# Optimization experiments

Hardware: AMD Instinct MI355X
Metric: run time of the kernel (lower is better)

The kernel has to match this reference:

```python
import jax, jax.numpy as jnp
import numpy as np

N_NODES = 20000   # N
N_EDGES = 320000  # E (avg degree 16)
T_STEPS = 16      # T
IN_FEATS = 1      # F
HG = 64           # hidden_g
HT = 128          # hidden_t
LN_EPS = 1e-5


def _layer_norm(x, g, b):
    mu = jnp.mean(x, axis=-1, keepdims=True)
    var = jnp.mean((x - mu) ** 2, axis=-1, keepdims=True)
    return (x - mu) * jax.lax.rsqrt(var + LN_EPS) * g + b


def setup_inputs() -> dict:
    key = jax.random.key(0)
    k = jax.random.split(key, 16)
    r = lambda i, shape, s: jax.random.normal(k[i], shape, jnp.float32) * s
    return dict(
        x_seq=jax.random.normal(k[0], (1, T_STEPS, N_NODES, IN_FEATS), jnp.float32),
        edge_index=jax.random.randint(k[1], (2, N_EDGES), 0, N_NODES, dtype=jnp.int32),
        # SAGEConv layer 0: lin_l (aggregated neighbors, has bias) + lin_r (root)
        W_l0=r(2, (IN_FEATS, HG), 0.5), W_r0=r(3, (IN_FEATS, HG), 0.5), b0=jnp.zeros((HG,), jnp.float32),
        ln0_g=jnp.ones((HG,), jnp.float32), ln0_b=jnp.zeros((HG,), jnp.float32),
        # SAGEConv layer 1
        W_l1=r(4, (HG, HG), 0.1), W_r1=r(5, (HG, HG), 0.1), b1=jnp.zeros((HG,), jnp.float32),
        ln1_g=jnp.ones((HG,), jnp.float32), ln1_b=jnp.zeros((HG,), jnp.float32),
        # GRU (torch layout: gates r,z,n stacked along first dim)
        gru_Wih=r(6, (3 * HT, HG), 0.05), gru_Whh=r(7, (3 * HT, HT), 0.05),
        gru_bih=jnp.zeros((3 * HT,), jnp.float32), gru_bhh=jnp.zeros((3 * HT,), jnp.float32),
        # head
        head_W=r(8, (HT, 1), 0.05), head_b=jnp.zeros((1,), jnp.float32),
    )


def reference(x_seq, edge_index, W_l0, W_r0, b0, ln0_g, ln0_b,
              W_l1, W_r1, b1, ln1_g, ln1_b,
              gru_Wih, gru_Whh, gru_bih, gru_bhh, head_W, head_b):
    src, dst = edge_index[0], edge_index[1]
    # in-degree for mean aggregation (clamped to 1, like PyG mean aggr on isolated nodes)
    deg = jnp.clip(jax.ops.segment_sum(jnp.ones((N_EDGES,), jnp.float32), dst,
                                       num_segments=N_NODES), 1.0)[:, None]

    def sage(x, Wl, Wr, b):
        # mean over incoming neighbors, then lin_l(aggr) + lin_r(root)
        agg = jax.ops.segment_sum(x[src], dst, num_segments=N_NODES) / deg
        return agg @ Wl + x @ Wr + b

    def stack(xt):  # xt: (N, F) -> (N, HG); dropout is identity in eval mode
        h = jax.nn.relu(_layer_norm(sage(xt, W_l0, W_r0, b0), ln0_g, ln0_b))
        h = jax.nn.relu(_layer_norm(sage(h, W_l1, W_r1, b1), ln1_g, ln1_b))
        return h

    X = x_seq[0]  # (T, N, F), B == 1
    # scan over timesteps (matches the per-t Python loop, bounds peak memory)
    _, H = jax.lax.scan(lambda c, xt: (c, stack(xt)), None, X)  # H: (T, N, HG)

    def gru_step(h, xt):  # torch GRU cell; batch = N nodes
        gi = xt @ gru_Wih.T + gru_bih
        gh = h @ gru_Whh.T + gru_bhh
        ir, iz, inn = jnp.split(gi, 3, axis=-1)
        hr, hz, hn = jnp.split(gh, 3, axis=-1)
        r = jax.nn.sigmoid(ir + hr)
        z = jax.nn.sigmoid(iz + hz)
        n = jnp.tanh(inn + r * hn)
        return (1.0 - z) * n + z * h, None

    h0 = jnp.zeros((N_NODES, HT), x_seq.dtype)
    hT, _ = jax.lax.scan(gru_step, h0, H)
    y = (hT @ head_W + head_b)[:, 0]  # (N,)
    return y
```

## Files before the change

### kernel.cpp

```cpp
#include <hip/hip_runtime.h>
#include <math.h>

#define NN 20000
#define NE 320000
#define TS 16
#define HG 64
#define HTT 128
#define NG 384
#define LN_EPS 1e-5f

typedef __attribute__((ext_vector_type(8))) _Float16 f16x8;
typedef __attribute__((ext_vector_type(4))) _Float16 f16x4;
typedef __attribute__((ext_vector_type(2))) _Float16 f16x2;
typedef __attribute__((ext_vector_type(4))) float f32x4;

__device__ __forceinline__ float wave_sum64(float v) {
  #pragma unroll
  for (int off = 32; off > 0; off >>= 1) v += __shfl_xor(v, off, 64);
  return v;
}
__device__ __forceinline__ float quad_sum16(float v) {
  #pragma unroll
  for (int off = 1; off < 16; off <<= 1) v += __shfl_xor(v, off, 64);
  return v;
}
__device__ __forceinline__ float fast_sigmoid(float x) {
  return __builtin_amdgcn_rcpf(1.f + __expf(-x));
}
__device__ __forceinline__ float fast_tanh(float x) {
  float e = __expf(-2.f * fabsf(x));
  float th = (1.f - e) * __builtin_amdgcn_rcpf(1.f + e);
  return copysignf(th, x);
}

__global__ __launch_bounds__(256) void k_setup(
    const float* __restrict__ x_seq, float* __restrict__ xT,
    const float* __restrict__ Wih, _Float16* __restrict__ WihF,
    const float* __restrict__ Whh, _Float16* __restrict__ WhhF,
    const float* __restrict__ Wl1, const float* __restrict__ Wr1,
    _Float16* __restrict__ Wchi, _Float16* __restrict__ Wclo,
    const float* __restrict__ Wl0, const float* __restrict__ Wr0,
    const float* __restrict__ b0, const float* __restrict__ g0,
    const float* __restrict__ be0, float* __restrict__ P,
    int* __restrict__ cnt) {
  int gid = blockIdx.x * 256 + threadIdx.x;
  int stride = gridDim.x * 256;
  for (int i = gid; i < NN * TS; i += stride) {
    int t = i / NN, n = i - t * NN;
    xT[n * 16 + t] = x_seq[i];
  }
  for (int i = gid; i < NG * HG; i += stride) WihF[i] = (_Float16)Wih[i];
  for (int i = gid; i < NG * HTT; i += stride) WhhF[i] = (_Float16)Whh[i];
  for (int i = gid; i < HG * 128; i += stride) {
    int n = i >> 7, k = i & 127;
    float x = (k < HG) ? Wl1[k * HG + n] : Wr1[(k - HG) * HG + n];
    _Float16 h = (_Float16)x;
    Wchi[i] = h;
    Wclo[i] = (_Float16)(x - (float)h);
  }
  for (int i = gid; i < NN; i += stride) cnt[i] = 0;
  if (blockIdx.x == 0 && threadIdx.x < 64) {
    int f = threadIdx.x;
    float u = Wl0[f], v = Wr0[f], c = b0[f], g = g0[f];
    float um = wave_sum64(u) * (1.f / 64.f);
    float vm = wave_sum64(v) * (1.f / 64.f);
    float cm = wave_sum64(c) * (1.f / 64.f);
    float uc = u - um, vc = v - vm, cc = c - cm;
    float muu = wave_sum64(uc * uc) * (1.f / 64.f);
    float mvv = wave_sum64(vc * vc) * (1.f / 64.f);
    float mcc = wave_sum64(cc * cc) * (1.f / 64.f);
    float muv = wave_sum64(uc * vc) * (1.f / 64.f);
    float muc = wave_sum64(uc * cc) * (1.f / 64.f);
    float mvc = wave_sum64(vc * cc) * (1.f / 64.f);
    P[f] = uc * g; P[64 + f] = vc * g; P[128 + f] = cc * g; P[192 + f] = be0[f];
    if (f == 0) {
      P[256] = muu; P[257] = mvv; P[258] = mcc;
      P[259] = muv; P[260] = muc; P[261] = mvc;
    }
  }
}

__global__ void k_hist(const int* __restrict__ dst, int* cnt) {
  int e = blockIdx.x * blockDim.x + threadIdx.x;
  if (e < NE) atomicAdd(&cnt[dst[e]], 1);
}

__global__ void k_scan(int* cnt, int* row_ptr, float* deg_inv) {
  __shared__ int s[1024];
  const int PER = 20;
  int tid = threadIdx.x;
  int base = tid * PER;
  int vloc[PER], dloc[PER];
  int sum = 0;
  #pragma unroll
  for (int j = 0; j < PER; j++) {
    int n = base + j;
    int d = (n < NN) ? cnt[n] : 0;
    vloc[j] = sum;
    dloc[j] = d;
    sum += d;
  }
  s[tid] = sum;
  __syncthreads();
  for (int off = 1; off < 1024; off <<= 1) {
    int t = (tid >= off) ? s[tid - off] : 0;
    __syncthreads();
    s[tid] += t;
    __syncthreads();
  }
  int excl = s[tid] - sum;
  #pragma unroll
  for (int j = 0; j < PER; j++) {
    int n = base + j;
    if (n < NN) {
      int rp = excl + vloc[j];
      row_ptr[n] = rp;
      cnt[n] = rp;
      int d = dloc[j];
      deg_inv[n] = 1.0f / (float)((d > 1) ? d : 1);
    }
  }
  if (tid == 1023) row_ptr[NN] = s[1023];
}

__global__ void k_fill(const int* __restrict__ src, const int* __restrict__ dst,
                       int* cursor, int* col) {
  int e = blockIdx.x * blockDim.x + threadIdx.x;
  if (e < NE) {
    int p = atomicAdd(&cursor[dst[e]], 1);
    col[p] = src[e];
  }
}

__global__ __launch_bounds__(256) void k_h0_fused(
    const float* __restrict__ xT,
    const int* __restrict__ row_ptr, const int* __restrict__ col,
    const float* __restrict__ deg_inv,
    const float* __restrict__ P,
    _Float16* __restrict__ h0r,
    _Float16* __restrict__ code2) {
  int lane = threadIdx.x & 63;
  int n = blockIdx.x * 4 + (threadIdx.x >> 6);
  int grp = lane >> 4, tl = lane & 15;
  int beg = row_ptr[n];
  int deg = row_ptr[n + 1] - beg;
  float s0 = 0.f, s1 = 0.f;
  int iters = (deg + 7) >> 3;
  for (int it = 0; it < iters; it++) {
    int e0 = it * 8 + grp, e1 = it * 8 + 4 + grp;
    bool v0 = e0 < deg, v1 = e1 < deg;
    int i0 = v0 ? e0 : 0, i1 = v1 ? e1 : 0;
    int c0 = col[beg + i0];
    int c1 = col[beg + i1];
    float x0 = xT[c0 * 16 + tl];
    float x1 = xT[c1 * 16 + tl];
    s0 += v0 ? x0 : 0.f;
    s1 += v1 ? x1 : 0.f;
  }
  float s = s0 + s1;
  s += __shfl_xor(s, 16, 64);
  s += __shfl_xor(s, 32, 64);
  float aggv = s * deg_inv[n];
  float xv = xT[n * 16 + tl];
  float muu = P[256], mvv = P[257], mcc = P[258];
  float muv = P[259], muc = P[260], mvc = P[261];
  if (lane < 16) {
    float a = aggv, x = xv;
    float var = a * a * muu + x * x * mvv + mcc
              + 2.f * (a * x * muv + a * muc + x * mvc);
    float rstd = rsqrtf(var + LN_EPS);
    _Float16 Ah = (_Float16)(a * rstd);
    _Float16 Xh = (_Float16)(x * rstd);
    _Float16 Ch = (_Float16)rstd;
    f16x8 cw = {Ah, Ah, Xh, Xh, Ch, Ch, (_Float16)0.f, (_Float16)0.f};
    *(f16x8*)&code2[(size_t)n * 128 + (lane & 7) * 16 + (lane >> 3) * 8] = cw;
  }
  #pragma unroll
  for (int half = 0; half < 2; half++) {
    int c = lane + half * 64;
    int t = c >> 3, f8 = (c & 7) * 8;
    float a = __shfl(aggv, t, 64);
    float x = __shfl(xv, t, 64);
    float var = a * a * muu + x * x * mvv + mcc
              + 2.f * (a * x * muv + a * muc + x * mvc);
    float rstd = rsqrtf(var + LN_EPS);
    f16x8 o;
    #pragma unroll
    for (int j = 0; j < 8; j++) {
      int f = f8 + j;
      float d = a * P[f] + x * P[64 + f] + P[128 + f];
      o[j] = (_Float16)fmaxf(d * rstd + P[192 + f], 0.f);
    }
    *(f16x8*)&h0r[(size_t)n * 1024 + c * 8] = o;
  }
}

__global__ __launch_bounds__(256) void k_gather(
    const int* __restrict__ row_ptr, const int* __restrict__ col,
    const _Float16* __restrict__ code2,
    const float* __restrict__ P,
    _Float16* __restrict__ agg) {
  int lane = threadIdx.x & 63;
  int n = blockIdx.x * 4 + (threadIdx.x >> 6);
  const f16x2 h2z = {(_Float16)0.f, (_Float16)0.f};
  const f16x2 h2o = {(_Float16)1.f, (_Float16)1.f};
  int f1 = (lane & 7) * 8;
  int tmod = lane >> 3;
  f16x2 Pu2[4], Pv2[4], Pc2[4], Pb2[4];
  #pragma unroll
  for (int j = 0; j < 4; j++) {
    Pu2[j] = (f16x2){(_Float16)P[f1 + 2*j],       (_Float16)P[f1 + 2*j + 1]};
    Pv2[j] = (f16x2){(_Float16)P[64 + f1 + 2*j],  (_Float16)P[64 + f1 + 2*j + 1]};
    Pc2[j] = (f16x2){(_Float16)P[128 + f1 + 2*j], (_Float16)P[128 + f1 + 2*j + 1]};
    Pb2[j] = (f16x2){(_Float16)P[192 + f1 + 2*j], (_Float16)P[192 + f1 + 2*j + 1]};
  }
  int beg = row_ptr[n];
  int deg = row_ptr[n + 1] - beg;
  int cvAll = (lane < deg) ? col[beg + lane] : 0;

  f16x2 aE1[4], aO1[4], aE2[4], aO2[4];
  #pragma unroll
  for (int j = 0; j < 4; j++) { aE1[j] = h2z; aO1[j] = h2z; aE2[j] = h2z; aO2[j] = h2z; }

#define ACC_SET(c, mk, FULL, ACC)                                          \
  { f16x2 _A = __builtin_shufflevector(c, c, 0, 1);                        \
    f16x2 _X = __builtin_shufflevector(c, c, 2, 3);                        \
    f16x2 _C = __builtin_shufflevector(c, c, 4, 5);                        \
    _Pragma("unroll")                                                      \
    for (int j = 0; j < 4; j++) {                                          \
      f16x2 d = __builtin_elementwise_fma(_A, Pu2[j],                      \
                 __builtin_elementwise_fma(_X, Pv2[j],                     \
                  __builtin_elementwise_fma(_C, Pc2[j], Pb2[j])));         \
      d = __builtin_elementwise_max(d, h2z);                               \
      ACC[j] = (FULL) ? (ACC[j] + d)                                       \
                      : __builtin_elementwise_fma(d, mk, ACC[j]);          \
    } }

  int nb4 = (deg + 3) >> 2;
  if (nb4 > 16) nb4 = 16;
  for (int b = 0; b < nb4; b++) {
    int eb = b << 2;
    f16x8 cA[4], cB[4];
    #pragma unroll
    for (int e = 0; e < 4; e++) {
      int c = __builtin_amdgcn_readlane(cvAll, eb + e);
      const _Float16* cp = code2 + (size_t)c * 128 + tmod * 16;
      cA[e] = *(const f16x8*)cp;
      cB[e] = *(const f16x8*)(cp + 8);
    }
    if (eb + 4 <= deg) {
      #pragma unroll
      for (int e = 0; e < 4; e++) {
        if (e & 1) { ACC_SET(cA[e], h2o, true, aO1) ACC_SET(cB[e], h2o, true, aO2) }
        else       { ACC_SET(cA[e], h2o, true, aE1) ACC_SET(cB[e], h2o, true, aE2) }
      }
    } else {
      #pragma unroll
      for (int e = 0; e < 4; e++) {
        f16x2 mk = ((eb + e) < deg) ? h2o : h2z;
        if (e & 1) { ACC_SET(cA[e], mk, false, aO1) ACC_SET(cB[e], mk, false, aO2) }
        else       { ACC_SET(cA[e], mk, false, aE1) ACC_SET(cB[e], mk, false, aE2) }
      }
    }
  }
  for (int e = 64; e < deg; e++) {
    int c = col[beg + e];
    const _Float16* cp = code2 + (size_t)c * 128 + tmod * 16;
    f16x8 ca = *(const f16x8*)cp;
    f16x8 cb = *(const f16x8*)(cp + 8);
    ACC_SET(ca, h2o, true, aE1) ACC_SET(cb, h2o, true, aE2)
  }
#undef ACC_SET

  float dif = 1.0f / (float)((deg > 1) ? deg : 1);
  _Float16 dih = (_Float16)dif;
  f16x2 di2 = {dih, dih};
  union { f16x8 v; f16x2 h[4]; } u0, u1;
  #pragma unroll
  for (int j = 0; j < 4; j++) {
    u0.h[j] = (aE1[j] + aO1[j]) * di2;
    u1.h[j] = (aE2[j] + aO2[j]) * di2;
  }
  *(f16x8*)&agg[(size_t)n * 1024 + lane * 8] = u0.v;
  *(f16x8*)&agg[(size_t)n * 1024 + 512 + lane * 8] = u1.v;
}

__global__ __launch_bounds__(256) void k_gemm(
    const _Float16* __restrict__ h0r,
    const _Float16* __restrict__ agg,
    const _Float16* __restrict__ Wchi, const _Float16* __restrict__ Wclo,
    const float* __restrict__ b1, const float* __restrict__ g1, const float* __restrict__ be1,
    _Float16* __restrict__ Ht_all) {
  int tid = threadIdx.x;
  int lane = tid & 63, wave = tid >> 6;
  int col16 = lane & 15, quad = lane >> 4;
  int m0 = blockIdx.x * 16;

  float bias[4], gg[4], bb[4];
  #pragma unroll
  for (int nt = 0; nt < 4; nt++) {
    int nf = nt * 16 + col16;
    bias[nt] = b1[nf]; gg[nt] = g1[nf]; bb[nt] = be1[nf];
  }
  size_t rowbase = (size_t)(m0 + col16) * 1024;

  for (int ts = 0; ts < 4; ts++) {
    int t = wave * 4 + ts;
    f32x4 acc[4];
    #pragma unroll
    for (int nt = 0; nt < 4; nt++) acc[nt] = (f32x4){0.f, 0.f, 0.f, 0.f};

    f16x8 aa[2], ar[2];
    #pragma unroll
    for (int kk = 0; kk < 2; kk++) {
      aa[kk] = *(const f16x8*)&agg[rowbase + t * 64 + kk * 32 + quad * 8];
      ar[kk] = *(const f16x8*)&h0r[rowbase + t * 64 + kk * 32 + quad * 8];
    }
    #pragma unroll
    for (int kk = 0; kk < 2; kk++) {
      #pragma unroll
      for (int nt = 0; nt < 4; nt++) {
        int nf = nt * 16 + col16;
        f16x8 bh = *(const f16x8*)&Wchi[nf * 128 + kk * 32 + quad * 8];
        f16x8 bl = *(const f16x8*)&Wclo[nf * 128 + kk * 32 + quad * 8];
        acc[nt] = __builtin_amdgcn_mfma_f32_16x16x32_f16(aa[kk], bh, acc[nt], 0, 0, 0);
        acc[nt] = __builtin_amdgcn_mfma_f32_16x16x32_f16(aa[kk], bl, acc[nt], 0, 0, 0);
      }
    }
    #pragma unroll
    for (int kk = 0; kk < 2; kk++) {
      #pragma unroll
      for (int nt = 0; nt < 4; nt++) {
        int nf = nt * 16 + col16;
        f16x8 bh = *(const f16x8*)&Wchi[nf * 128 + 64 + kk * 32 + quad * 8];
        f16x8 bl = *(const f16x8*)&Wclo[nf * 128 + 64 + kk * 32 + quad * 8];
        acc[nt] = __builtin_amdgcn_mfma_f32_16x16x32_f16(ar[kk], bh, acc[nt], 0, 0, 0);
        acc[nt] = __builtin_amdgcn_mfma_f32_16x16x32_f16(ar[kk], bl, acc[nt], 0, 0, 0);
      }
    }

    #pragma unroll
    for (int r = 0; r < 4; r++) {
      float v[4];
      #pragma unroll
      for (int nt = 0; nt < 4; nt++) v[nt] = acc[nt][r] + bias[nt];
      float s = (v[0] + v[1]) + (v[2] + v[3]);
      float mu = quad_sum16(s) * (1.f / 64.f);
      float sq = 0.f;
      #pragma unroll
      for (int nt = 0; nt < 4; nt++) { v[nt] -= mu; sq += v[nt] * v[nt]; }
      float var = quad_sum16(sq) * (1.f / 64.f);
      float rstd = rsqrtf(var + LN_EPS);
      int m = m0 + quad * 4 + r;
      size_t base = ((size_t)t * NN + m) * HG;
      #pragma unroll
      for (int nt = 0; nt < 4; nt++) {
        float o = fmaxf(v[nt] * rstd * gg[nt] + bb[nt], 0.f);
        Ht_all[base + nt * 16 + col16] = (_Float16)o;
      }
    }
  }
}

__global__ __launch_bounds__(256, 2) void k_gru_all(
    const _Float16* __restrict__ Ht_all,
    const _Float16* __restrict__ WihF,
    const _Float16* __restrict__ WhhF,
    const float* __restrict__ bih, const float* __restrict__ bhh,
    const float* __restrict__ headW, const float* __restrict__ headb,
    float* __restrict__ out) {
  __shared__ _Float16 WihL[NG * 64];
  __shared__ _Float16 hL[2][32 * 128];
  __shared__ float yL[4][32];

  int tid = threadIdx.x;
  int lane = tid & 63, wave = tid >> 6;
  int col16 = lane & 15, quad = lane >> 4;
  int m0 = blockIdx.x * 32;
  int gb = 2 * wave;

  for (int i = tid; i < NG * 8; i += 256) {
    int g = i >> 3, k8 = i & 7;
    *(f16x8*)&WihL[g * 64 + ((k8 + g) & 7) * 8] = *(const f16x8*)&WihF[g * 64 + k8 * 8];
  }
  for (int i = tid; i < 2 * 32 * 128; i += 256) hL[0][i] = (_Float16)0.f;

  int gts[6];
  #pragma unroll
  for (int t6 = 0; t6 < 6; t6++)
    gts[t6] = (t6 < 2) ? (gb + t6) : (t6 < 4) ? (8 + gb + t6 - 2) : (16 + gb + t6 - 4);

  f16x8 wgh[4][6];
  #pragma unroll
  for (int kk = 0; kk < 4; kk++)
    #pragma unroll
    for (int t6 = 0; t6 < 6; t6++)
      wgh[kk][t6] = *(const f16x8*)&WhhF[(size_t)(gts[t6] * 16 + col16) * HTT + kk * 32 + quad * 8];

  int jj[2]; float bR[2], bZ[2], bNi[2], bNh[2], hw[2];
  int waddr[2][4][2];
  #pragma unroll
  for (int js = 0; js < 2; js++) {
    int j = (gb + js) * 16 + col16;
    jj[js] = j;
    bR[js]  = bih[j] + bhh[j];
    bZ[js]  = bih[HTT + j] + bhh[HTT + j];
    bNi[js] = bih[2 * HTT + j];
    bNh[js] = bhh[2 * HTT + j];
    hw[js]  = headW[j];
    #pragma unroll
    for (int mt = 0; mt < 2; mt++)
      #pragma unroll
      for (int r = 0; r < 4; r++) {
        int row = mt * 16 + quad * 4 + r;
        waddr[mt][r][js] = row * 128 + (((j >> 3) + row) & 15) * 8 + (j & 7);
      }
  }
  float hreg[2][4][2];
  #pragma unroll
  for (int mt = 0; mt < 2; mt++)
    #pragma unroll
    for (int r = 0; r < 4; r++) { hreg[mt][r][0] = 0.f; hreg[mt][r][1] = 0.f; }

  size_t aoff[2][2];
  #pragma unroll
  for (int kk = 0; kk < 2; kk++)
    #pragma unroll
    for (int mt = 0; mt < 2; mt++)
      aoff[kk][mt] = (size_t)(m0 + mt * 16 + col16) * HG + kk * 32 + quad * 8;

  __syncthreads();

  for (int t = 0; t < TS; t++) {
    const _Float16* hcur = hL[t & 1];
    _Float16* hnxt = hL[(t + 1) & 1];

    f32x4 acc[8][2];
    #pragma unroll
    for (int a = 0; a < 8; a++) {
      acc[a][0] = (f32x4){0.f, 0.f, 0.f, 0.f};
      acc[a][1] = (f32x4){0.f, 0.f, 0.f, 0.f};
    }

    const _Float16* AH = Ht_all + (size_t)t * NN * HG;
    f16x8 gah[2][2];
    #pragma unroll
    for (int kk = 0; kk < 2; kk++)
      #pragma unroll
      for (int mt = 0; mt < 2; mt++)
        gah[kk][mt] = *(const f16x8*)&AH[aoff[kk][mt]];

    #pragma unroll
    for (int kk = 0; kk < 4; kk++) {
      f16x8 ah[2];
      #pragma unroll
      for (int mt = 0; mt < 2; mt++) {
        int row = mt * 16 + col16;
        int k8 = kk * 4 + quad;
        ah[mt] = *(const f16x8*)&hcur[row * 128 + ((k8 + row) & 15) * 8];
      }
      #pragma unroll
      for (int t6 = 0; t6 < 6; t6++) {
        int ai = (t6 < 4) ? t6 : t6 + 2;
        #pragma unroll
        for (int mt = 0; mt < 2; mt++)
          acc[ai][mt] = __builtin_amdgcn_mfma_f32_16x16x32_f16(ah[mt], wgh[kk][t6], acc[ai][mt], 0, 0, 0);
      }
    }
    #pragma unroll
    for (int kk = 0; kk < 2; kk++) {
      #pragma unroll
      for (int t6 = 0; t6 < 6; t6++) {
        int g = gts[t6] * 16 + col16;
        int k8 = kk * 4 + quad;
        f16x8 b = *(const f16x8*)&WihL[g * 64 + ((k8 + g) & 7) * 8];
        #pragma unroll
        for (int mt = 0; mt < 2; mt++)
          acc[t6][mt] = __builtin_amdgcn_mfma_f32_16x16x32_f16(gah[kk][mt], b, acc[t6][mt], 0, 0, 0);
      }
    }

    #pragma unroll
    for (int mt = 0; mt < 2; mt++) {
      #pragma unroll
      for (int r = 0; r < 4; r++) {
        #pragma unroll
        for (int js = 0; js < 2; js++) {
          float R  = acc[0 + js][mt][r] + bR[js];
          float Z  = acc[2 + js][mt][r] + bZ[js];
          float Ni = acc[4 + js][mt][r] + bNi[js];
          float Nh = acc[6 + js][mt][r] + bNh[js];
          float rg = fast_sigmoid(R);
          float zg = fast_sigmoid(Z);
          float nn = fast_tanh(Ni + rg * Nh);
          float hn = nn + zg * (hreg[mt][r][js] - nn);
          hreg[mt][r][js] = hn;
          hnxt[waddr[mt][r][js]] = (_Float16)hn;
        }
      }
    }
    __syncthreads();
  }

  #pragma unroll
  for (int mt = 0; mt < 2; mt++) {
    #pragma unroll
    for (int r = 0; r < 4; r++) {
      float py = hreg[mt][r][0] * hw[0] + hreg[mt][r][1] * hw[1];
      py = quad_sum16(py);
      if (col16 == 0) yL[wave][mt * 16 + quad * 4 + r] = py;
    }
  }
  __syncthreads();
  if (tid < 32)
    out[m0 + tid] = yL[0][tid] + yL[1][tid] + yL[2][tid] + yL[3][tid] + headb[0];
}

extern "C" void kernel_launch(void* const* d_in, const int* in_sizes, int n_in,
                              void* d_out, int out_size, void* d_ws, size_t ws_size,
                              hipStream_t stream) {
  const float* x_seq = (const float*)d_in[0];
  const int*   edge  = (const int*)d_in[1];
  const float* Wl0   = (const float*)d_in[2];
  const float* Wr0   = (const float*)d_in[3];
  const float* b0    = (const float*)d_in[4];
  const float* g0    = (const float*)d_in[5];
  const float* be0   = (const float*)d_in[6];
  const float* Wl1   = (const float*)d_in[7];
  const float* Wr1   = (const float*)d_in[8];
  const float* b1    = (const float*)d_in[9];
  const float* g1    = (const float*)d_in[10];
  const float* be1   = (const float*)d_in[11];
  const float* Wih   = (const float*)d_in[12];
  const float* Whh   = (const float*)d_in[13];
  const float* bih   = (const float*)d_in[14];
  const float* bhh   = (const float*)d_in[15];
  const float* headW = (const float*)d_in[16];
  const float* headb = (const float*)d_in[17];
  float* out = (float*)d_out;

  const int* srcp = edge;
  const int* dstp = edge + NE;

  char* ws = (char*)d_ws;
  size_t off = 0;
  auto alloc = [&](size_t bytes) -> void* {
    void* p = ws + off;
    off += (bytes + 255) & ~(size_t)255;
    return p;
  };
  int*   cnt     = (int*)alloc(NN * 4);
  int*   row_ptr = (int*)alloc((NN + 1) * 4);
  int*   col     = (int*)alloc(NE * 4);
  float* deg_inv = (float*)alloc(NN * 4);
  float* xT      = (float*)alloc((size_t)NN * TS * 4);
  float* P       = (float*)alloc(512 * 4);
  _Float16* h0r  = (_Float16*)alloc((size_t)NN * 1024 * 2);
  _Float16* code2= (_Float16*)alloc((size_t)NN * 128 * 2);
  _Float16* agg  = (_Float16*)alloc((size_t)NN * 1024 * 2);
  _Float16* Ht_all = (_Float16*)alloc((size_t)TS * NN * HG * 2);
  _Float16* WihF = (_Float16*)alloc((size_t)NG * HG * 2);
  _Float16* WhhF = (_Float16*)alloc((size_t)NG * HTT * 2);
  _Float16* Wchi = (_Float16*)alloc((size_t)HG * 128 * 2);
  _Float16* Wclo = (_Float16*)alloc((size_t)HG * 128 * 2);
  (void)ws_size; (void)in_sizes; (void)n_in; (void)out_size;

  k_setup<<<1250, 256, 0, stream>>>(x_seq, xT, Wih, WihF, Whh, WhhF,
                                    Wl1, Wr1, Wchi, Wclo,
                                    Wl0, Wr0, b0, g0, be0, P, cnt);
  k_hist<<<(NE + 255) / 256, 256, 0, stream>>>(dstp, cnt);
  k_scan<<<1, 1024, 0, stream>>>(cnt, row_ptr, deg_inv);
  k_fill<<<(NE + 255) / 256, 256, 0, stream>>>(srcp, dstp, cnt, col);
  k_h0_fused<<<NN / 4, 256, 0, stream>>>(xT, row_ptr, col, deg_inv, P, h0r, code2);
  k_gather<<<NN / 4, 256, 0, stream>>>(row_ptr, col, code2, P, agg);
  k_gemm<<<NN / 16, 256, 0, stream>>>(h0r, agg, Wchi, Wclo, b1, g1, be1, Ht_all);
  k_gru_all<<<NN / 32, 256, 0, stream>>>(Ht_all, WihF, WhhF, bih, bhh,
                                         headW, headb, out);
}
```

Measured before the change: 364.8 us.

## Double-buffer neighbor code loads and drop GRU Wih LDS staging for occupancy

In the aggregation kernel, the gather of neighbor code rows is software-pipelined so the next block of four edges is loaded while the current block is accumulated. In the GRU kernel, the 48KB LDS copy of Wih is removed and B fragments are read straight from global memory through cache, with launch bounds raised to 4 blocks per CU. Lower LDS use should allow more resident blocks and better latency hiding. The cost is extra registers for the doubled buffers and global/L2 traffic on every timestep's Wih reads, which could cause spills at the tighter register budget.

```diff
diff --git a/kernel.cpp b/kernel.cpp
--- a/kernel.cpp
+++ b/kernel.cpp
@@ -236,31 +236,45 @@
                       : __builtin_elementwise_fma(d, mk, ACC[j]);          \
     } }
 
+#define LOADBLK(CA, CB, EB)                                                \
+  { _Pragma("unroll")                                                      \
+    for (int e = 0; e < 4; e++) {                                          \
+      int c = __builtin_amdgcn_readlane(cvAll, (EB) + e);                  \
+      const _Float16* cp = code2 + (size_t)c * 128 + tmod * 16;            \
+      CA[e] = *(const f16x8*)cp;                                           \
+      CB[e] = *(const f16x8*)(cp + 8);                                     \
+    } }
+
+#define ACCBLK(CA, CB, EB)                                                 \
+  { if ((EB) + 4 <= deg) {                                                 \
+      _Pragma("unroll")                                                    \
+      for (int e = 0; e < 4; e++) {                                        \
+        if (e & 1) { ACC_SET(CA[e], h2o, true, aO1) ACC_SET(CB[e], h2o, true, aO2) } \
+        else       { ACC_SET(CA[e], h2o, true, aE1) ACC_SET(CB[e], h2o, true, aE2) } \
+      }                                                                    \
+    } else {                                                               \
+      _Pragma("unroll")                                                    \
+      for (int e = 0; e < 4; e++) {                                        \
+        f16x2 mk = (((EB) + e) < deg) ? h2o : h2z;                         \
+        if (e & 1) { ACC_SET(CA[e], mk, false, aO1) ACC_SET(CB[e], mk, false, aO2) } \
+        else       { ACC_SET(CA[e], mk, false, aE1) ACC_SET(CB[e], mk, false, aE2) } \
+      }                                                                    \
+    } }
+
   int nb4 = (deg + 3) >> 2;
   if (nb4 > 16) nb4 = 16;
-  for (int b = 0; b < nb4; b++) {
-    int eb = b << 2;
-    f16x8 cA[4], cB[4];
-    #pragma unroll
-    for (int e = 0; e < 4; e++) {
-      int c = __builtin_amdgcn_readlane(cvAll, eb + e);
-      const _Float16* cp = code2 + (size_t)c * 128 + tmod * 16;
-      cA[e] = *(const f16x8*)cp;
-      cB[e] = *(const f16x8*)(cp + 8);
-    }
-    if (eb + 4 <= deg) {
-      #pragma unroll
-      for (int e = 0; e < 4; e++) {
-        if (e & 1) { ACC_SET(cA[e], h2o, true, aO1) ACC_SET(cB[e], h2o, true, aO2) }
-        else       { ACC_SET(cA[e], h2o, true, aE1) ACC_SET(cB[e], h2o, true, aE2) }
-      }
-    } else {
-      #pragma unroll
-      for (int e = 0; e < 4; e++) {
-        f16x2 mk = ((eb + e) < deg) ? h2o : h2z;
-        if (e & 1) { ACC_SET(cA[e], mk, false, aO1) ACC_SET(cB[e], mk, false, aO2) }
-        else       { ACC_SET(cA[e], mk, false, aE1) ACC_SET(cB[e], mk, false, aE2) }
-      }
+  {
+    f16x8 cA[4], cB[4], nA[4], nB[4];
+    if (nb4 > 0) LOADBLK(cA, cB, 0)
+    int b = 0;
+    while (b < nb4) {
+      if (b + 1 < nb4) LOADBLK(nA, nB, (b + 1) << 2)
+      ACCBLK(cA, cB, b << 2)
+      b++;
+      if (b >= nb4) break;
+      if (b + 1 < nb4) LOADBLK(cA, cB, (b + 1) << 2)
+      ACCBLK(nA, nB, b << 2)
+      b++;
     }
   }
   for (int e = 64; e < deg; e++) {
@@ -270,6 +284,8 @@
     f16x8 cb = *(const f16x8*)(cp + 8);
     ACC_SET(ca, h2o, true, aE1) ACC_SET(cb, h2o, true, aE2)
   }
+#undef ACCBLK
+#undef LOADBLK
 #undef ACC_SET
 
   float dif = 1.0f / (float)((deg > 1) ? deg : 1);
@@ -362,14 +378,13 @@
   }
 }
 
-__global__ __launch_bounds__(256, 2) void k_gru_all(
+__global__ __launch_bounds__(256, 4) void k_gru_all(
     const _Float16* __restrict__ Ht_all,
     const _Float16* __restrict__ WihF,
     const _Float16* __restrict__ WhhF,
     const float* __restrict__ bih, const float* __restrict__ bhh,
     const float* __restrict__ headW, const float* __restrict__ headb,
     float* __restrict__ out) {
-  __shared__ _Float16 WihL[NG * 64];
   __shared__ _Float16 hL[2][32 * 128];
   __shared__ float yL[4][32];
 
@@ -379,10 +394,6 @@
   int m0 = blockIdx.x * 32;
   int gb = 2 * wave;
 
-  for (int i = tid; i < NG * 8; i += 256) {
-    int g = i >> 3, k8 = i & 7;
-    *(f16x8*)&WihL[g * 64 + ((k8 + g) & 7) * 8] = *(const f16x8*)&WihF[g * 64 + k8 * 8];
-  }
   for (int i = tid; i < 2 * 32 * 128; i += 256) hL[0][i] = (_Float16)0.f;
 
   int gts[6];
@@ -397,12 +408,11 @@
     for (int t6 = 0; t6 < 6; t6++)
       wgh[kk][t6] = *(const f16x8*)&WhhF[(size_t)(gts[t6] * 16 + col16) * HTT + kk * 32 + quad * 8];
 
-  int jj[2]; float bR[2], bZ[2], bNi[2], bNh[2], hw[2];
+  float bR[2], bZ[2], bNi[2], bNh[2], hw[2];
   int waddr[2][4][2];
   #pragma unroll
   for (int js = 0; js < 2; js++) {
     int j = (gb + js) * 16 + col16;
-    jj[js] = j;
     bR[js]  = bih[j] + bhh[j];
     bZ[js]  = bih[HTT + j] + bhh[HTT + j];
     bNi[js] = bih[2 * HTT + j];
@@ -429,6 +439,13 @@
     for (int mt = 0; mt < 2; mt++)
       aoff[kk][mt] = (size_t)(m0 + mt * 16 + col16) * HG + kk * 32 + quad * 8;
 
+  size_t woff[2][6];
+  #pragma unroll
+  for (int kk = 0; kk < 2; kk++)
+    #pragma unroll
+    for (int t6 = 0; t6 < 6; t6++)
+      woff[kk][t6] = (size_t)(gts[t6] * 16 + col16) * 64 + (kk * 4 + quad) * 8;
+
   __syncthreads();
 
   for (int t = 0; t < TS; t++) {
@@ -471,9 +488,7 @@
     for (int kk = 0; kk < 2; kk++) {
       #pragma unroll
       for (int t6 = 0; t6 < 6; t6++) {
-        int g = gts[t6] * 16 + col16;
-        int k8 = kk * 4 + quad;
-        f16x8 b = *(const f16x8*)&WihL[g * 64 + ((k8 + g) & 7) * 8];
+        f16x8 b = *(const f16x8*)&WihF[woff[kk][t6]];
         #pragma unroll
         for (int mt = 0; mt < 2; mt++)
           acc[t6][mt] = __builtin_amdgcn_mfma_f32_16x16x32_f16(gah[kk][mt], b, acc[t6][mt], 0, 0, 0);
```

Result: slower. 657.7 us (+80.3%).
